# Performance work log

Measured on AMD Instinct MI355X. Metric: run time of the kernel, lower is better.

The kernel has to match this reference:

```python
import jax, jax.numpy as jnp
import numpy as np


def conv1x1(x, w, b):
    # x: [B,Cin,H,W], w: [Cout,Cin], b: [Cout]
    return jnp.einsum('bchw,oc->bohw', x, w) + b[None, :, None, None]


def _lin_idx_w(in_size, out_size):
    # PyTorch bilinear, align_corners=False: src = max((i+0.5)*scale - 0.5, 0)
    scale = in_size / out_size
    src = jnp.maximum((jnp.arange(out_size, dtype=jnp.float32) + 0.5) * scale - 0.5, 0.0)
    i0 = jnp.floor(src).astype(jnp.int32)
    i0 = jnp.minimum(i0, in_size - 1)
    i1 = jnp.minimum(i0 + 1, in_size - 1)
    w1 = src - i0.astype(jnp.float32)
    return i0, i1, w1


def bilinear_resize(x, out_h, out_w):
    Hin, Win = x.shape[-2], x.shape[-1]
    y0, y1, wy = _lin_idx_w(Hin, out_h)
    x0, x1, wx = _lin_idx_w(Win, out_w)
    wy = wy[:, None]  # [out_h,1]
    rows = x[:, :, y0, :] * (1.0 - wy) + x[:, :, y1, :] * wy
    out = rows[:, :, :, x0] * (1.0 - wx) + rows[:, :, :, x1] * wx      # [B,C,out_h,out_w]
    return out


def setup_inputs() -> dict:
    key = jax.random.key(0)
    ks = jax.random.split(key, 10)
    C, C8 = 512, 64
    s = 1.0 / np.sqrt(C)
    return {
        'content': jax.random.normal(ks[0], (4, C, 64, 64), jnp.float32),
        'style': jax.random.normal(ks[1], (4, C, 80, 80), jnp.float32),
        'f_w': jax.random.normal(ks[2], (C8, C), jnp.float32) * s,
        'f_b': jax.random.normal(ks[3], (C8,), jnp.float32) * 0.01,
        'g_w': jax.random.normal(ks[4], (C8, C), jnp.float32) * s,
        'g_b': jax.random.normal(ks[5], (C8,), jnp.float32) * 0.01,
        'h_w': jax.random.normal(ks[6], (C, C), jnp.float32) * s,
        'h_b': jax.random.normal(ks[7], (C,), jnp.float32) * 0.01,
        'out_w': jax.random.normal(ks[8], (C, C), jnp.float32) * s,
        'out_b': jax.random.normal(ks[9], (C,), jnp.float32) * 0.01,
    }


def reference(content, style, f_w, f_b, g_w, g_b, h_w, h_b, out_w, out_b):
    B, C, H, W = content.shape
    HW = H * W
    f = conv1x1(content, f_w, f_b).reshape(B, -1, HW)                       # [B,C8,HW] (query, pre-transpose)
    g = bilinear_resize(conv1x1(style, g_w, g_b), H, W).reshape(B, -1, HW)  # [B,C8,HW]
    h = bilinear_resize(conv1x1(style, h_w, h_b), H, W).reshape(B, C, HW)   # [B,C,HW]
    attn = jax.nn.softmax(jnp.einsum('bcm,bcn->bmn', f, g), axis=-1)        # [B,HW_q,HW_k]
    out = jnp.einsum('bcn,bmn->bcm', h, attn).reshape(B, C, H, W)
    return conv1x1(out, out_w, out_b)
```

## Files before the change

kernel.cpp:

```cpp
#include <hip/hip_runtime.h>

#define NB 4
#define NC 512
#define ND 64
#define HW 4096
#define SPIN 6400

typedef _Float16 f16;
typedef _Float16 f16x8 __attribute__((ext_vector_type(8)));
typedef short s16x8 __attribute__((ext_vector_type(8)));
typedef short s16x4 __attribute__((ext_vector_type(4)));
typedef float f32x4 __attribute__((ext_vector_type(4)));
typedef float f32x16 __attribute__((ext_vector_type(16)));
typedef unsigned short ushortT;

__device__ __forceinline__ unsigned short f32_to_bf16(float x) {
  union { float f; unsigned u; } v; v.f = x;
  unsigned r = v.u + 0x7FFFu + ((v.u >> 16) & 1u);
  return (unsigned short)(r >> 16);
}

__device__ __forceinline__ void stv(float* p, float v) { *p = v; }
__device__ __forceinline__ void stv(f16* p, float v) { *p = (f16)v; }
__device__ __forceinline__ void stv(unsigned short* p, float v) { *p = f32_to_bf16(v); }

__device__ __forceinline__ unsigned cvt_pk_bf16(float lo, float hi) {
  unsigned r;
  asm("v_cvt_pk_bf16_f32 %0, %1, %2" : "=v"(r) : "v"(lo), "v"(hi));
  return r;
}

__global__ __launch_bounds__(256) void cvtw_kernel(const float* __restrict__ fw,
                                                   const float* __restrict__ gw,
                                                   const float* __restrict__ hw,
                                                   const float* __restrict__ ow,
                                                   f16* __restrict__ dst) {
  int i = blockIdx.x * 256 + threadIdx.x;
  const float* src; int off;
  if (i < 32768) { src = fw; off = 0; }
  else if (i < 65536) { src = gw; off = 32768; }
  else if (i < 327680) { src = hw; off = 65536; }
  else { src = ow; off = 327680; }
  dst[i] = (f16)src[i - off];
}

__global__ __launch_bounds__(256) void tcvt_kernel(const float* __restrict__ in,
                                                   f16* __restrict__ out) {
  __shared__ float Xs[64][65];
  int p0 = blockIdx.x * 64, c0 = blockIdx.y * 64, b = blockIdx.z;
  int t = threadIdx.x;
  const float* ib = in + ((size_t)b * NC + c0) * HW + p0;
  int pl = t & 63, cg = t >> 6;
#pragma unroll
  for (int k = 0; k < 16; ++k) {
    int c = cg * 16 + k;
    Xs[c][pl] = ib[(size_t)c * HW + pl];
  }
  __syncthreads();
  int p = t >> 2, cb = (t & 3) * 16;
  union { f16 h[16]; float4 q[2]; } u;
#pragma unroll
  for (int j = 0; j < 16; ++j) u.h[j] = (f16)Xs[cb + j][p];
  f16* ob = out + ((size_t)b * HW + p0 + p) * NC + c0 + cb;
  *(float4*)(ob) = u.q[0];
  *(float4*)(ob + 8) = u.q[1];
}

__global__ __launch_bounds__(256) void rstcvt_kernel(const float* __restrict__ X,
                                                     f16* __restrict__ Y) {
  __shared__ float Xs[64 * 165];
  int oy = blockIdx.x, c0 = blockIdx.y * 64, b = blockIdx.z;
  float syf = fmaxf((oy + 0.5f) * 1.25f - 0.5f, 0.f);
  int y0 = (int)syf; int y1 = min(y0 + 1, 79); float wy = syf - (float)y0;
  int t = threadIdx.x;
  const float* Xb = X + ((size_t)b * NC + c0) * SPIN;
#pragma unroll
  for (int k = 0; k < 10; ++k) {
    int idx = t + k * 256;
    int c = idx / 40;
    int rem = idx - c * 40;
    int yy = rem / 20;
    int x4 = rem - yy * 20;
    int ysrc = yy ? y1 : y0;
    float4 v = *(const float4*)(Xb + (size_t)c * SPIN + ysrc * 80 + x4 * 4);
    float* d = Xs + c * 165 + yy * 82 + x4 * 4;
    d[0] = v.x; d[1] = v.y; d[2] = v.z; d[3] = v.w;
  }
  __syncthreads();
  int ox = t >> 2, cb = (t & 3) * 16;
  float sxf = fmaxf((ox + 0.5f) * 1.25f - 0.5f, 0.f);
  int x0 = (int)sxf; int x1 = min(x0 + 1, 79); float wx = sxf - (float)x0;
  union { f16 h[16]; float4 q[2]; } u;
#pragma unroll
  for (int j = 0; j < 16; ++j) {
    const float* base = Xs + (cb + j) * 165;
    float a0 = base[x0], a1 = base[x1];
    float b0 = base[82 + x0], b1 = base[82 + x1];
    float r0 = a0 + (a1 - a0) * wx;
    float r1 = b0 + (b1 - b0) * wx;
    u.h[j] = (f16)(r0 + (r1 - r0) * wy);
  }
  f16* ob = Y + ((size_t)b * HW + oy * 64 + ox) * NC + c0 + cb;
  *(float4*)(ob) = u.q[0];
  *(float4*)(ob + 8) = u.q[1];
}

__global__ __launch_bounds__(256) void convpm2_kernel(const f16* __restrict__ X0,
                                                      const f16* __restrict__ X1,
                                                      const f16* __restrict__ W01,
                                                      const float* __restrict__ b0,
                                                      const float* __restrict__ b1,
                                                      f16* __restrict__ Y0,
                                                      f16* __restrict__ Y1) {
  int sel = blockIdx.z >> 2;
  int b = blockIdx.z & 3;
  const f16* X = sel ? X1 : X0;
  const f16* W = W01 + sel * (ND * NC);
  const float* bias = sel ? b1 : b0;
  f16* Y = sel ? Y1 : Y0;
  int t = threadIdx.x, l = t & 63, w = t >> 6;
  int pw = blockIdx.x * 256 + w * 64;
  int l4 = l & 15, g = l >> 4;
  f32x4 acc[4][4] = {};
  const f16* Xb = X + ((size_t)b * HW + pw) * NC;
  for (int kk = 0; kk < 16; ++kk) {
    int co = kk * 32 + g * 8;
    f16x8 a[4], bb[4];
#pragma unroll
    for (int ms = 0; ms < 4; ++ms) a[ms] = *(const f16x8*)(Xb + (size_t)(ms * 16 + l4) * NC + co);
#pragma unroll
    for (int ct = 0; ct < 4; ++ct) bb[ct] = *(const f16x8*)(W + (size_t)(ct * 16 + l4) * NC + co);
#pragma unroll
    for (int ms = 0; ms < 4; ++ms)
#pragma unroll
      for (int ct = 0; ct < 4; ++ct)
        acc[ms][ct] = __builtin_amdgcn_mfma_f32_16x16x32_f16(a[ms], bb[ct], acc[ms][ct], 0, 0, 0);
  }
  float bv[4];
#pragma unroll
  for (int ct = 0; ct < 4; ++ct) bv[ct] = bias[ct * 16 + l4];
  f16* Yb = Y + ((size_t)b * HW + pw) * ND;
#pragma unroll
  for (int ms = 0; ms < 4; ++ms)
#pragma unroll
    for (int ct = 0; ct < 4; ++ct)
#pragma unroll
      for (int r = 0; r < 4; ++r)
        Yb[(size_t)(ms * 16 + g * 4 + r) * ND + ct * 16 + l4] = (f16)(acc[ms][ct][r] + bv[ct]);
}

template <typename OUT_T>
__global__ __launch_bounds__(256) void convcm_kernel(const f16* __restrict__ X,
                                                     const f16* __restrict__ W,
                                                     const float* __restrict__ bias,
                                                     OUT_T* __restrict__ Y, int O) {
  int b = blockIdx.z;
  int o0 = blockIdx.x * 64;
  int t = threadIdx.x, l = t & 63, w = t >> 6;
  int pw = blockIdx.y * 256 + w * 64;
  int l4 = l & 15, g = l >> 4;
  f32x4 acc[4][4] = {};
  const f16* Xb = X + ((size_t)b * HW + pw) * NC;
  const f16* Wb = W + (size_t)o0 * NC;
  for (int kk = 0; kk < 16; ++kk) {
    int co = kk * 32 + g * 8;
    f16x8 a[4], bb[4];
#pragma unroll
    for (int ms = 0; ms < 4; ++ms) a[ms] = *(const f16x8*)(Wb + (size_t)(ms * 16 + l4) * NC + co);
#pragma unroll
    for (int ct = 0; ct < 4; ++ct) bb[ct] = *(const f16x8*)(Xb + (size_t)(ct * 16 + l4) * NC + co);
#pragma unroll
    for (int ms = 0; ms < 4; ++ms)
#pragma unroll
      for (int ct = 0; ct < 4; ++ct)
        acc[ms][ct] = __builtin_amdgcn_mfma_f32_16x16x32_f16(a[ms], bb[ct], acc[ms][ct], 0, 0, 0);
  }
  float bv[4][4];
#pragma unroll
  for (int ms = 0; ms < 4; ++ms)
#pragma unroll
    for (int r = 0; r < 4; ++r) bv[ms][r] = bias[o0 + ms * 16 + g * 4 + r];
#pragma unroll
  for (int ms = 0; ms < 4; ++ms)
#pragma unroll
    for (int ct = 0; ct < 4; ++ct)
#pragma unroll
      for (int r = 0; r < 4; ++r) {
        float val = acc[ms][ct][r] + bv[ms][r];
        stv(&Y[((size_t)b * O + o0 + ms * 16 + g * 4 + r) * HW + pw + ct * 16 + l4], val);
      }
}

union PAu { unsigned u[4]; s16x8 v; };
union VSu { s16x8 v; s16x4 h[2]; };

__global__ __launch_bounds__(256, 2) void attn_kernel(const f16* __restrict__ FT,
                                                      const f16* __restrict__ GT,
                                                      const unsigned short* __restrict__ HC,
                                                      f16* __restrict__ MIDT) {
  __shared__ __align__(16) char Vs[2][32768];
  int bid = blockIdx.x;
  int b = (bid & 7) >> 1;
  int cs = bid & 1;
  int mt = bid >> 3;
  int t = threadIdx.x, l = t & 63, w = t >> 6;
  int lm = l & 31, hf = l >> 5;
  int mf = w >> 1, cq = w & 1;
  int mr = mt * 64 + mf * 32;
  int cqb = cq * 128;

  const f16* Fq = FT + ((size_t)b * HW + mr + lm) * ND + hf * 8;
  f16x8 q[4];
#pragma unroll
  for (int kc = 0; kc < 4; ++kc) q[kc] = *(const f16x8*)(Fq + kc * 16);

  const f16* kp = GT + (size_t)b * HW * ND + (size_t)lm * ND + hf * 8;

  int sc = t >> 3;
  int nseg = (t & 7) * 8;
  int sb0 = ((nseg >> 4) * 32) + (((nseg >> 3) & 1) * 8);
  const unsigned short* vsrc =
      HC + ((size_t)b * NC + cs * 256 + sc) * HW + nseg;

  f32x16 acc[4] = {};
  float den = 0.f;

  const int cl0 = cqb + lm;
  const int vsw = (lm & 7) << 4;

#define STAGE_LOAD(n0x)                                                   \
  do {                                                                    \
    _Pragma("unroll") for (int r_ = 0; r_ < 8; ++r_)                      \
        vreg[r_].v = *(const s16x8*)(vsrc + (size_t)r_ * 32 * HW + (n0x)); \
  } while (0)

#define STAGE_WRITE(bufidx)                                               \
  do {                                                                    \
    _Pragma("unroll") for (int r_ = 0; r_ < 8; ++r_) {                    \
      int cl_ = r_ * 32 + sc;                                             \
      char* row_ = Vs[bufidx] + cl_ * 128;                                \
      int sw_ = (cl_ & 7) << 4;                                           \
      *(s16x4*)(row_ + (sb0 ^ sw_)) = vreg[r_].h[0];                      \
      *(s16x4*)(row_ + ((sb0 + 16) ^ sw_)) = vreg[r_].h[1];               \
    }                                                                     \
  } while (0)

#define PACK(sv, PA, o)                                                   \
  do {                                                                    \
    float p_[16];                                                         \
    _Pragma("unroll") for (int r_ = 0; r_ < 16; ++r_) {                   \
      p_[r_] = __expf(sv[r_]);                                            \
      den += p_[r_];                                                      \
    }                                                                     \
    PA[o].u[0] = cvt_pk_bf16(p_[0], p_[1]);                               \
    PA[o].u[1] = cvt_pk_bf16(p_[2], p_[3]);                               \
    PA[o].u[2] = cvt_pk_bf16(p_[4], p_[5]);                               \
    PA[o].u[3] = cvt_pk_bf16(p_[6], p_[7]);                               \
    PA[o + 1].u[0] = cvt_pk_bf16(p_[8], p_[9]);                           \
    PA[o + 1].u[1] = cvt_pk_bf16(p_[10], p_[11]);                         \
    PA[o + 1].u[2] = cvt_pk_bf16(p_[12], p_[13]);                         \
    PA[o + 1].u[3] = cvt_pk_bf16(p_[14], p_[15]);                         \
  } while (0)

#define PVBODY(PA, Vc)                                                    \
  do {                                                                    \
    s16x8 vb_[4], vn_[4];                                                 \
    _Pragma("unroll") for (int kn = 0; kn < 4; ++kn)                      \
        vb_[kn] = *(const s16x8*)((Vc) + cl0 * 128 + ((kn * 32 + hf * 16) ^ vsw)); \
    _Pragma("unroll") for (int cf = 0; cf < 4; ++cf) {                    \
      if (cf < 3) {                                                       \
        const char* vr_ = (Vc) + (cl0 + (cf + 1) * 32) * 128;             \
        _Pragma("unroll") for (int kn = 0; kn < 4; ++kn)                  \
            vn_[kn] = *(const s16x8*)(vr_ + ((kn * 32 + hf * 16) ^ vsw)); \
      }                                                                   \
      __builtin_amdgcn_s_setprio(1);                                      \
      _Pragma("unroll") for (int kn = 0; kn < 4; ++kn)                    \
          acc[cf] = __builtin_amdgcn_mfma_f32_32x32x16_bf16(PA[kn].v, vb_[kn], acc[cf], 0, 0, 0); \
      __builtin_amdgcn_s_setprio(0);                                      \
      if (cf < 3) {                                                       \
        _Pragma("unroll") for (int kn = 0; kn < 4; ++kn) vb_[kn] = vn_[kn]; \
      }                                                                   \
    }                                                                     \
  } while (0)

#define ITER(IT, PC, PP, KC, KN, DOPV)                                    \
  do {                                                                    \
    const int n0 = (IT) * 64;                                             \
    VSu vreg[8];                                                          \
    if ((IT) < 63) {                                                      \
      STAGE_LOAD(n0 + 64);                                                \
      _Pragma("unroll") for (int h_ = 0; h_ < 2; ++h_)                    \
          _Pragma("unroll") for (int kc = 0; kc < 4; ++kc)                \
          KN[h_][kc] = *(const f16x8*)(kp + (size_t)(n0 + 64 + h_ * 32) * ND + kc * 16); \
    }                                                                     \
    f32x16 s0 = {}, s1 = {};                                              \
    _Pragma("unroll") for (int kc = 0; kc < 4; ++kc)                      \
        s0 = __builtin_amdgcn_mfma_f32_32x32x16_f16(KC[0][kc], q[kc], s0, 0, 0, 0); \
    _Pragma("unroll") for (int kc = 0; kc < 4; ++kc)                      \
        s1 = __builtin_amdgcn_mfma_f32_32x32x16_f16(KC[1][kc], q[kc], s1, 0, 0, 0); \
    if (DOPV) {                                                           \
      const char* Vc_ = Vs[((IT) + 1) & 1];              \
      PVBODY(PP, Vc_);                                                    \
    }                                                                     \
    PACK(s0, PC, 0);                                                      \
    PACK(s1, PC, 2);                                                      \
    __syncthreads();                                                      \
    if ((IT) < 63) STAGE_WRITE(((IT) + 1) & 1);                           \
  } while (0)

  {
    VSu vreg[8];
    STAGE_LOAD(0);
    STAGE_WRITE(0);
  }
  f16x8 kbP[2][4], kbQ[2][4];
#pragma unroll
  for (int h = 0; h < 2; ++h)
#pragma unroll
    for (int kc = 0; kc < 4; ++kc)
      kbP[h][kc] = *(const f16x8*)(kp + (size_t)(h * 32) * ND + kc * 16);
  __syncthreads();

  PAu paA[4], paB[4];
  ITER(0, paA, paB, kbP, kbQ, false);
  for (int ito = 1; ito < 63; ito += 2) {
    ITER(ito, paB, paA, kbQ, kbP, true);
    ITER(ito + 1, paA, paB, kbP, kbQ, true);
  }
  ITER(63, paB, paA, kbQ, kbP, true);
  PVBODY(paB, (const char*)Vs[1]);

#undef STAGE_LOAD
#undef STAGE_WRITE
#undef PACK
#undef PVBODY
#undef ITER

  den += __shfl_xor(den, 32);
  float rd = 1.f / den;
  f16* Mb = MIDT + ((size_t)b * HW + mr) * NC + cs * 256 + cqb + lm;
#pragma unroll
  for (int r = 0; r < 16; ++r) {
    int mrow = (r & 3) + 8 * (r >> 2) + 4 * hf;
    float rv = __shfl(rd, mrow);
#pragma unroll
    for (int cf = 0; cf < 4; ++cf)
      Mb[(size_t)mrow * NC + cf * 32] = (f16)(acc[cf][r] * rv);
  }
}

extern "C" void kernel_launch(void* const* d_in, const int* in_sizes, int n_in,
                              void* d_out, int out_size, void* d_ws, size_t ws_size,
                              hipStream_t stream) {
  const float* content = (const float*)d_in[0];
  const float* style   = (const float*)d_in[1];
  const float* f_w = (const float*)d_in[2];
  const float* f_b = (const float*)d_in[3];
  const float* g_w = (const float*)d_in[4];
  const float* g_b = (const float*)d_in[5];
  const float* h_w = (const float*)d_in[6];
  const float* h_b = (const float*)d_in[7];
  const float* out_w = (const float*)d_in[8];
  const float* out_b = (const float*)d_in[9];
  float* out = (float*)d_out;

  const size_t MB = 1ull << 20;
  char* base = (char*)d_ws;
  f16* contentT = (f16*)base;
  f16* midT     = (f16*)base;
  unsigned short* hC = (unsigned short*)(base + 16 * MB);
  f16* fT = (f16*)(base + 32 * MB);
  f16* gT = (f16*)(base + 34 * MB);
  f16* styrT = (f16*)(base + 48 * MB);
  f16* w16 = (f16*)(base + 64 * MB);
  f16* fw16 = w16;
  f16* gw16 = w16 + 32768;
  f16* hw16 = w16 + 65536;
  f16* ow16 = w16 + 327680;

  cvtw_kernel<<<dim3(589824 / 256), 256, 0, stream>>>(f_w, g_w, h_w, out_w, w16);
  tcvt_kernel<<<dim3(HW / 64, NC / 64, NB), 256, 0, stream>>>(content, contentT);
  rstcvt_kernel<<<dim3(64, NC / 64, NB), 256, 0, stream>>>(style, styrT);
  convpm2_kernel<<<dim3(HW / 256, 1, 2 * NB), 256, 0, stream>>>(contentT, styrT, fw16, f_b, g_b, fT, gT);
  convcm_kernel<unsigned short><<<dim3(NC / 64, HW / 256, NB), 256, 0, stream>>>(styrT, hw16, h_b, hC, NC);
  attn_kernel<<<dim3(512), 256, 0, stream>>>(fT, gT, hC, midT);
  convcm_kernel<float><<<dim3(NC / 64, HW / 256, NB), 256, 0, stream>>>(midT, ow16, out_b, out, NC);
}
```

Baseline: 276.4 us.

## Stage X tiles through swizzled double-buffered LDS in channel-major 1x1 conv

The convcm kernel now loads X for the block's 256 pixels in 64-channel chunks with coalesced 16-byte reads, writing them into a 64KB double-buffered LDS tile with an XOR swizzle to avoid bank conflicts. Waves then read their MFMA B operands from LDS instead of issuing strided per-row global loads. Launch bounds now request two blocks per CU. The cost is 64KB of LDS per block and two barriers per chunk, which limits occupancy. The second barrier also makes the double buffer serialize rather than overlap.

Measured after the change: 267.7 us. -3.2%, faster.

```diff
diff --git a/kernel.cpp b/kernel.cpp
--- a/kernel.cpp
+++ b/kernel.cpp
@@ -150,31 +150,60 @@
 }
 
 template <typename OUT_T>
-__global__ __launch_bounds__(256) void convcm_kernel(const f16* __restrict__ X,
-                                                     const f16* __restrict__ W,
-                                                     const float* __restrict__ bias,
-                                                     OUT_T* __restrict__ Y, int O) {
+__global__ __launch_bounds__(256, 2) void convcm_kernel(const f16* __restrict__ X,
+                                                        const f16* __restrict__ W,
+                                                        const float* __restrict__ bias,
+                                                        OUT_T* __restrict__ Y, int O) {
+  __shared__ __align__(16) char Xs[2][32768];
   int b = blockIdx.z;
   int o0 = blockIdx.x * 64;
   int t = threadIdx.x, l = t & 63, w = t >> 6;
-  int pw = blockIdx.y * 256 + w * 64;
+  int pw0 = blockIdx.y * 256;
+  int pw = pw0 + w * 64;
   int l4 = l & 15, g = l >> 4;
   f32x4 acc[4][4] = {};
-  const f16* Xb = X + ((size_t)b * HW + pw) * NC;
+  const f16* Xb = X + ((size_t)b * HW + pw0) * NC;
   const f16* Wb = W + (size_t)o0 * NC;
-  for (int kk = 0; kk < 16; ++kk) {
-    int co = kk * 32 + g * 8;
-    f16x8 a[4], bb[4];
-#pragma unroll
-    for (int ms = 0; ms < 4; ++ms) a[ms] = *(const f16x8*)(Wb + (size_t)(ms * 16 + l4) * NC + co);
-#pragma unroll
-    for (int ct = 0; ct < 4; ++ct) bb[ct] = *(const f16x8*)(Xb + (size_t)(ct * 16 + l4) * NC + co);
-#pragma unroll
-    for (int ms = 0; ms < 4; ++ms)
+
+  int ps = t >> 3, ccs = t & 7;
+  const f16* xsrc = Xb + (size_t)ps * NC + ccs * 8;
+  char* xw = Xs[0] + ps * 128 + ((ccs * 16) ^ ((ps & 7) << 4));
+
+  const int rsw = (l4 & 7) << 4;
+  const char* xrd = Xs[0] + (w * 64 + l4) * 128;
+
+  for (int cn = 0; cn < 8; ++cn) {
+    const int boff = (cn & 1) * 32768;
+#pragma unroll
+    for (int h = 0; h < 2; ++h) {
+      s16x8 xreg[4];
+#pragma unroll
+      for (int r = 0; r < 4; ++r)
+        xreg[r] = *(const s16x8*)(xsrc + (size_t)((h * 4 + r) * 32) * NC + cn * 64);
+#pragma unroll
+      for (int r = 0; r < 4; ++r)
+        *(s16x8*)(xw + boff + (h * 4 + r) * 4096) = xreg[r];
+    }
+    __syncthreads();
+#pragma unroll
+    for (int kk2 = 0; kk2 < 2; ++kk2) {
+      int co = cn * 64 + kk2 * 32 + g * 8;
+      f16x8 a[4], bb[4];
+#pragma unroll
+      for (int ms = 0; ms < 4; ++ms)
+        a[ms] = *(const f16x8*)(Wb + (size_t)(ms * 16 + l4) * NC + co);
 #pragma unroll
       for (int ct = 0; ct < 4; ++ct)
-        acc[ms][ct] = __builtin_amdgcn_mfma_f32_16x16x32_f16(a[ms], bb[ct], acc[ms][ct], 0, 0, 0);
-  }
+        bb[ct] = *(const f16x8*)(xrd + boff + ct * 2048 + ((kk2 * 64 + g * 16) ^ rsw));
+#pragma unroll
+      for (int ms = 0; ms < 4; ++ms)
+#pragma unroll
+        for (int ct = 0; ct < 4; ++ct)
+          acc[ms][ct] = __builtin_amdgcn_mfma_f32_16x16x32_f16(a[ms], bb[ct], acc[ms][ct], 0, 0, 0);
+    }
+    __syncthreads();
+  }
+
   float bv[4][4];
 #pragma unroll
   for (int ms = 0; ms < 4; ++ms)
```
